# Optimization experiments

Measured on AMD Instinct MI355X. Metric: run time of the kernel, lower is better.

The kernel has to match this reference:

```python
import jax, jax.numpy as jnp
import numpy as np

N_NODES = 100000
N_EDGES = 1600000
D_IN = 128
D_HID = 128
D_OUT = 128


def setup_inputs() -> dict:
    key = jax.random.key(0)
    ks = jax.random.split(key, 6)
    node_features = jax.random.normal(ks[0], (N_NODES, D_IN), dtype=jnp.float32)
    edge_index = jax.random.randint(ks[1], (2, N_EDGES), 0, N_NODES, dtype=jnp.int32)
    s1 = 1.0 / np.sqrt(D_IN)
    s2 = 1.0 / np.sqrt(D_HID)
    W1 = jax.random.normal(ks[2], (D_IN, D_HID), dtype=jnp.float32) * s1
    W2 = jax.random.normal(ks[3], (D_HID, D_HID), dtype=jnp.float32) * s2
    W3 = jax.random.normal(ks[4], (D_HID, D_OUT), dtype=jnp.float32) * s2
    b1 = jnp.zeros((D_HID,), dtype=jnp.float32)
    b2 = jnp.zeros((D_HID,), dtype=jnp.float32)
    b3 = jnp.zeros((D_OUT,), dtype=jnp.float32)
    return {"node_features": node_features, "edge_index": edge_index,
            "W1": W1, "b1": b1, "W2": W2, "b2": b2, "W3": W3, "b3": b3}


def _aggregate(x, src, dst, n_nodes):
    # mean over incoming neighbors (by dst), residual add; degree clamped to >=1
    msg = jax.ops.segment_sum(x[src], dst, num_segments=n_nodes)  # [N, D]
    deg = jax.ops.segment_sum(jnp.ones_like(dst, dtype=x.dtype), dst,
                              num_segments=n_nodes)
    deg = jnp.maximum(deg, 1.0)[:, None]
    return x + msg / deg


def reference(node_features, edge_index, W1, b1, W2, b2, W3, b3):
    n_nodes = node_features.shape[0]
    src, dst = edge_index[0], edge_index[1]
    x = _aggregate(node_features, src, dst, n_nodes)
    x = jax.nn.relu(x @ W1 + b1)
    x = _aggregate(x, src, dst, n_nodes)
    x = jax.nn.relu(x @ W2 + b2)
    x = x.mean(axis=0)  # graph readout -> [D_HID]
    return x @ W3 + b3  # [D_OUT]
```

## Files before the change

kernel.cpp:

```cpp
#include <hip/hip_runtime.h>

#define D 128
#define SLOTS 64
#define NB 391
#define NBANK 8
#define SUBCAP 768
#define BINCAP (NBANK * SUBCAP)
#define BATCH 2048
#define EPB 8
#define CNTSTRIDE 16
#define WPITCH 136

typedef __attribute__((ext_vector_type(8))) short short8;
typedef __attribute__((ext_vector_type(4))) float float4v;

__device__ inline unsigned short f2bf(float f) {
    union { float f; unsigned u; } a; a.f = f;
    unsigned u = a.u;
    return (unsigned short)((u + 0x7fffu + ((u >> 16) & 1u)) >> 16);
}
__device__ inline unsigned packbf(float a, float b) {
    return (unsigned)f2bf(a) | ((unsigned)f2bf(b) << 16);
}
__device__ inline unsigned pack4fp8(float a, float b, float c, float d) {
    int t = __builtin_amdgcn_cvt_pk_fp8_f32(a, b, 0, false);
    t = __builtin_amdgcn_cvt_pk_fp8_f32(c, d, t, true);
    return (unsigned)t;
}
__device__ inline unsigned char pack1fp8(float a) {
    int t = __builtin_amdgcn_cvt_pk_fp8_f32(a, 0.f, 0, false);
    return (unsigned char)(t & 0xff);
}
__device__ inline void acc8fp8(float* acc, uint2 w) {
    auto f0 = __builtin_amdgcn_cvt_pk_f32_fp8(w.x, false);
    auto f1 = __builtin_amdgcn_cvt_pk_f32_fp8(w.x, true);
    auto f2 = __builtin_amdgcn_cvt_pk_f32_fp8(w.y, false);
    auto f3 = __builtin_amdgcn_cvt_pk_f32_fp8(w.y, true);
    acc[0] += f0[0]; acc[1] += f0[1]; acc[2] += f1[0]; acc[3] += f1[1];
    acc[4] += f2[0]; acc[5] += f2[1]; acc[6] += f3[0]; acc[7] += f3[1];
}


__global__ __launch_bounds__(256) void k_head(const int* __restrict__ src,
                                              const int* __restrict__ dst, int nE,
                                              int* __restrict__ gcnt, int* __restrict__ bins,
                                              const float* __restrict__ x,
                                              unsigned char* __restrict__ y8,
                                              unsigned char* __restrict__ h8dummy,
                                              float* __restrict__ colsum,
                                              int n16, int nBatches) {
    __shared__ int hist[512];
    __shared__ int excl[512];
    __shared__ int base[NB];
    __shared__ int stage[BATCH];
    __shared__ int gofs[BATCH];
    __shared__ int waveSum[4];
    int tid = threadIdx.x;

    if (blockIdx.x >= nBatches) {
        int cb = blockIdx.x - nBatches;
        if (cb == 0) {
            if (tid < 128) colsum[tid] = 0.f;
            else if (tid < 136)
                reinterpret_cast<uint4*>(y8)[(size_t)n16 + (tid - 128)] = make_uint4(0, 0, 0, 0);
            else if (tid < 144)
                reinterpret_cast<uint4*>(h8dummy)[tid - 136] = make_uint4(0, 0, 0, 0);
        }
        int i = cb * 256 + tid;
        if (i < n16) {
            const float4* xin = reinterpret_cast<const float4*>(x) + (size_t)i * 4;
            float4 v0 = xin[0], v1 = xin[1], v2 = xin[2], v3 = xin[3];
            uint4 o;
            o.x = pack4fp8(v0.x, v0.y, v0.z, v0.w);
            o.y = pack4fp8(v1.x, v1.y, v1.z, v1.w);
            o.z = pack4fp8(v2.x, v2.y, v2.z, v2.w);
            o.w = pack4fp8(v3.x, v3.y, v3.z, v3.w);
            reinterpret_cast<uint4*>(y8)[i] = o;
        }
        return;
    }

    int start = blockIdx.x * BATCH;
    int cntB = nE - start; if (cntB > BATCH) cntB = BATCH;
    if (cntB <= 0) return;
    int bank = blockIdx.x & (NBANK - 1);

    hist[tid] = 0; hist[tid + 256] = 0;
    __syncthreads();

    int b[EPB], r[EPB], v[EPB];
    #pragma unroll
    for (int i = 0; i < EPB; ++i) {
        int e = start + i * 256 + tid;
        if (e < nE) {
            int d = dst[e];
            b[i] = d >> 8;
            v[i] = (src[e] << 8) | (d & 255);
            r[i] = atomicAdd(&hist[b[i]], 1);
        } else b[i] = -1;
    }
    __syncthreads();

    int e0 = tid * 2, e1 = e0 + 1;
    int h0 = hist[e0], h1v = hist[e1];
    int s = h0 + h1v;
    int lane = tid & 63, w = tid >> 6;
    int sum = s;
    #pragma unroll
    for (int off2 = 1; off2 < 64; off2 <<= 1) {
        int tmp = __shfl_up(sum, off2, 64);
        if (lane >= off2) sum += tmp;
    }
    if (lane == 63) waveSum[w] = sum;
    __syncthreads();
    int wbase = 0;
    if (w > 0) wbase += waveSum[0];
    if (w > 1) wbase += waveSum[1];
    if (w > 2) wbase += waveSum[2];
    int exclPair = wbase + sum - s;
    excl[e0] = exclPair;
    excl[e1] = exclPair + h0;
    if (tid < NB)
        base[tid] = atomicAdd(&gcnt[(tid * NBANK + bank) * CNTSTRIDE], hist[tid]);
    if (tid + 256 < NB)
        base[tid + 256] = atomicAdd(&gcnt[((tid + 256) * NBANK + bank) * CNTSTRIDE], hist[tid + 256]);
    __syncthreads();

    #pragma unroll
    for (int i = 0; i < EPB; ++i) {
        if (b[i] >= 0) {
            int p = excl[b[i]] + r[i];
            int o = base[b[i]] + r[i];
            stage[p] = v[i];
            gofs[p] = (o < SUBCAP) ? (b[i] * BINCAP + bank * SUBCAP + o) : -1;
        }
    }
    __syncthreads();

    #pragma unroll
    for (int i = 0; i < EPB; ++i) {
        int p = i * 256 + tid;
        if (p < cntB) {
            int g = gofs[p];
            if (g >= 0) bins[g] = stage[p];
        }
    }
}


__global__ __launch_bounds__(256) void k_scatter2(const int* __restrict__ gcnt,
                                                  const int* __restrict__ bins,
                                                  int* __restrict__ slots,
                                                  int* __restrict__ deg, int n, int nAll) {
    __shared__ int slotsL[128 * SLOTS];
    __shared__ int cntL[128];
    __shared__ int cnt8s[128];
    int tid = threadIdx.x;
    int bin = blockIdx.x >> 1;
    int half = blockIdx.x & 1;
    if (tid < 128) cntL[tid] = 0;
    __syncthreads();

    #pragma unroll
    for (int k = 0; k < NBANK; ++k) {
        int c = gcnt[(bin * NBANK + k) * CNTSTRIDE]; if (c > SUBCAP) c = SUBCAP;
        const int* eb = bins + (size_t)bin * BINCAP + k * SUBCAP;
        for (int i = tid; i < c; i += 256) {
            int vv = eb[i];
            int dl = vv & 255;
            if ((dl >> 7) == half) {
                int p = atomicAdd(&cntL[dl & 127], 1);
                if (p < SLOTS) slotsL[(dl & 127) * SLOTS + p] = vv >> 8;
            }
        }
    }
    __syncthreads();

    int node0 = bin * 256 + half * 128;
    int remNodes = n - node0;
    if (remNodes > 128) remNodes = 128;
    if (remNodes < 0) remNodes = 0;

    if (tid < remNodes) {
        int dg = cntL[tid]; if (dg > SLOTS) dg = SLOTS;
        int dgr = (dg + 7) & ~7;
        for (int p = dg; p < dgr; ++p) slotsL[tid * SLOTS + p] = nAll;
        deg[node0 + tid] = dg;
        cnt8s[tid] = dgr;
    }
    __syncthreads();

    uint4* gout = reinterpret_cast<uint4*>(slots + (size_t)node0 * SLOTS);
    const uint4* lin = reinterpret_cast<const uint4*>(slotsL);
    int nv = remNodes * (SLOTS / 4);
    for (int i = tid; i < nv; i += 256) {
        int nd = i >> 4, vec = i & 15;
        if ((vec << 2) < cnt8s[nd]) gout[i] = lin[i];
    }
}


__global__ void k_agg(const unsigned char* __restrict__ Xin8,
                      unsigned short* __restrict__ Xout,
                      const int* __restrict__ deg, const int* __restrict__ slots, int n) {
    int t = blockIdx.x * 256 + threadIdx.x;
    int node = t >> 4;
    int lane = t & 15;
    if (node >= n) return;
    int dg = deg[node];
    int cnt8 = (dg + 7) & ~7;
    float acc[8] = {0.f, 0.f, 0.f, 0.f, 0.f, 0.f, 0.f, 0.f};
    const int* sl = slots + (size_t)node * SLOTS;
    for (int j = 0; j < cnt8; j += 8) {
        int4 s4a = *reinterpret_cast<const int4*>(sl + j);
        int4 s4b = *reinterpret_cast<const int4*>(sl + j + 4);
        uint2 w0 = *reinterpret_cast<const uint2*>(Xin8 + (size_t)s4a.x * D + lane * 8);
        uint2 w1 = *reinterpret_cast<const uint2*>(Xin8 + (size_t)s4a.y * D + lane * 8);
        uint2 w2 = *reinterpret_cast<const uint2*>(Xin8 + (size_t)s4a.z * D + lane * 8);
        uint2 w3 = *reinterpret_cast<const uint2*>(Xin8 + (size_t)s4a.w * D + lane * 8);
        uint2 w4 = *reinterpret_cast<const uint2*>(Xin8 + (size_t)s4b.x * D + lane * 8);
        uint2 w5 = *reinterpret_cast<const uint2*>(Xin8 + (size_t)s4b.y * D + lane * 8);
        uint2 w6 = *reinterpret_cast<const uint2*>(Xin8 + (size_t)s4b.z * D + lane * 8);
        uint2 w7 = *reinterpret_cast<const uint2*>(Xin8 + (size_t)s4b.w * D + lane * 8);
        acc8fp8(acc, w0); acc8fp8(acc, w1); acc8fp8(acc, w2); acc8fp8(acc, w3);
        acc8fp8(acc, w4); acc8fp8(acc, w5); acc8fp8(acc, w6); acc8fp8(acc, w7);
    }
    float inv = 1.0f / (float)(dg > 0 ? dg : 1);
    uint2 s8 = *reinterpret_cast<const uint2*>(Xin8 + (size_t)node * D + lane * 8);
    float self[8] = {0.f, 0.f, 0.f, 0.f, 0.f, 0.f, 0.f, 0.f};
    acc8fp8(self, s8);
    float o[8];
    #pragma unroll
    for (int k = 0; k < 8; ++k) o[k] = self[k] + acc[k] * inv;
    uint4 ov;
    ov.x = packbf(o[0], o[1]); ov.y = packbf(o[2], o[3]);
    ov.z = packbf(o[4], o[5]); ov.w = packbf(o[6], o[7]);
    reinterpret_cast<uint4*>(Xout + (size_t)node * D)[lane] = ov;
}


__global__ __launch_bounds__(256) void k_gemm(const unsigned short* __restrict__ X,
                                              const float* __restrict__ W,
                                              const float* __restrict__ bias,
                                              unsigned char* __restrict__ Y8,
                                              float* __restrict__ colsum,
                                              int n, int mode) {
    __shared__ unsigned short Wt[128 * WPITCH];
    __shared__ float cs[128];
    int tid = threadIdx.x;
    int wave = tid >> 6, L = tid & 63;
    int m16 = L & 15, g = L >> 4;

    #pragma unroll
    for (int i = 0; i < 8; ++i) {
        int p = i * 256 + tid;
        int col = p & 127, kg = p >> 7;
        unsigned pk[4];
        #pragma unroll
        for (int h = 0; h < 4; ++h) {
            float w0 = W[(kg * 8 + 2 * h + 0) * 128 + col];
            float w1 = W[(kg * 8 + 2 * h + 1) * 128 + col];
            pk[h] = packbf(w0, w1);
        }
        *reinterpret_cast<uint4*>(&Wt[col * WPITCH + kg * 8]) =
            make_uint4(pk[0], pk[1], pk[2], pk[3]);
    }
    if (mode && tid < 128) cs[tid] = 0.f;
    __syncthreads();

    int row0 = blockIdx.x * 128 + wave * 32;
    float4v zero4 = {0.f, 0.f, 0.f, 0.f};
    float4v acc[2][8];
    #pragma unroll
    for (int rt = 0; rt < 2; ++rt)
        #pragma unroll
        for (int ct = 0; ct < 8; ++ct) acc[rt][ct] = zero4;

    #pragma unroll
    for (int q = 0; q < 4; ++q) {
        int k0 = q * 32;
        short8 a[2];
        #pragma unroll
        for (int rt = 0; rt < 2; ++rt) {
            int row = row0 + rt * 16 + m16;
            short8 af = {0, 0, 0, 0, 0, 0, 0, 0};
            if (row < n)
                af = *reinterpret_cast<const short8*>(X + (size_t)row * D + k0 + g * 8);
            a[rt] = af;
        }
        #pragma unroll
        for (int ct = 0; ct < 8; ++ct) {
            short8 b = *reinterpret_cast<const short8*>(&Wt[(ct * 16 + m16) * WPITCH + k0 + g * 8]);
            acc[0][ct] = __builtin_amdgcn_mfma_f32_16x16x32_bf16(a[0], b, acc[0][ct], 0, 0, 0);
            acc[1][ct] = __builtin_amdgcn_mfma_f32_16x16x32_bf16(a[1], b, acc[1][ct], 0, 0, 0);
        }
    }

    float bj[8];
    #pragma unroll
    for (int ct = 0; ct < 8; ++ct) bj[ct] = bias[ct * 16 + m16];

    if (mode == 0) {
        #pragma unroll
        for (int rt = 0; rt < 2; ++rt)
            #pragma unroll
            for (int i = 0; i < 4; ++i) {
                int row = row0 + rt * 16 + g * 4 + i;
                if (row < n) {
                    #pragma unroll
                    for (int ct = 0; ct < 8; ++ct) {
                        float v = fmaxf(acc[rt][ct][i] + bj[ct], 0.f);
                        Y8[(size_t)row * D + ct * 16 + m16] = pack1fp8(v);
                    }
                }
            }
    } else {
        float csv[8] = {0.f, 0.f, 0.f, 0.f, 0.f, 0.f, 0.f, 0.f};
        #pragma unroll
        for (int rt = 0; rt < 2; ++rt)
            #pragma unroll
            for (int i = 0; i < 4; ++i) {
                int row = row0 + rt * 16 + g * 4 + i;
                if (row < n) {
                    #pragma unroll
                    for (int ct = 0; ct < 8; ++ct)
                        csv[ct] += fmaxf(acc[rt][ct][i] + bj[ct], 0.f);
                }
            }
        #pragma unroll
        for (int ct = 0; ct < 8; ++ct) atomicAdd(&cs[ct * 16 + m16], csv[ct]);
        __syncthreads();
        if (tid < 128) atomicAdd(&colsum[tid], cs[tid]);
    }
}


__global__ void k_final(const float* __restrict__ colsum, const float* __restrict__ W3,
                        const float* __restrict__ b3, float* __restrict__ out, float invN) {
    int j = threadIdx.x;
    float acc = b3[j];
    #pragma unroll 8
    for (int k = 0; k < D; ++k)
        acc += colsum[k] * invN * W3[k * D + j];
    out[j] = acc;
}


extern "C" void kernel_launch(void* const* d_in, const int* in_sizes, int n_in,
                              void* d_out, int out_size, void* d_ws, size_t ws_size,
                              hipStream_t stream) {
    const float* nf = (const float*)d_in[0];
    const int*   ei = (const int*)d_in[1];
    const float* W1 = (const float*)d_in[2];
    const float* b1 = (const float*)d_in[3];
    const float* W2 = (const float*)d_in[4];
    const float* b2 = (const float*)d_in[5];
    const float* W3 = (const float*)d_in[6];
    const float* b3 = (const float*)d_in[7];
    float* out = (float*)d_out;

    int n  = in_sizes[0] / D;
    int nE = in_sizes[1] / 2;
    const int* src = ei;
    const int* dst = ei + nE;

    int nBins = (n + 255) / 256;
    int nBatches = (nE + BATCH - 1) / BATCH;
    int n16 = n * (D / 16);

    char* ws = (char*)d_ws;
    size_t off = 0;
    auto alloc = [&](size_t bytes) -> void* {
        off = (off + 255) & ~(size_t)255;
        void* p = ws + off;
        off += bytes;
        return p;
    };
    int* gcnt  = (int*)alloc((size_t)nBins * NBANK * CNTSTRIDE * 4);
    int* bins  = (int*)alloc((size_t)nBins * BINCAP * 4);
    int* slots = (int*)alloc((size_t)nBins * 256 * SLOTS * 4);
    int* deg   = (int*)alloc((size_t)n * 4);
    unsigned char*  x8  = (unsigned char*) alloc((size_t)(n + 1) * D);
    unsigned short* t16 = (unsigned short*)alloc((size_t)n * D * 2);
    unsigned char*  h8  = (unsigned char*) alloc((size_t)(n + 1) * D);
    float* colsum = (float*)alloc(128 * 4);

    hipMemsetAsync(gcnt, 0, (size_t)nBins * NBANK * CNTSTRIDE * 4, stream);

    int gC = (n16 + 255) / 256;
    int gA = (n * 16 + 255) / 256;
    int gG = (n + 127) / 128;

    k_head<<<nBatches + gC, 256, 0, stream>>>(src, dst, nE, gcnt, bins,
                                              nf, x8, h8 + (size_t)n * D,
                                              colsum, n16, nBatches);
    k_scatter2<<<nBins * 2, 256, 0, stream>>>(gcnt, bins, slots, deg, n, n);

    k_agg<<<gA, 256, 0, stream>>>(x8, t16, deg, slots, n);
    k_gemm<<<gG, 256, 0, stream>>>(t16, W1, b1, h8, (float*)nullptr, n, 0);
    k_agg<<<gA, 256, 0, stream>>>(h8, t16, deg, slots, n);
    k_gemm<<<gG, 256, 0, stream>>>(t16, W2, b2, (unsigned char*)nullptr, colsum, n, 1);
    k_final<<<1, 128, 0, stream>>>(colsum, W3, b3, out, 1.0f / (float)n);
}
```

Before: 250.1 us.

## Halve bucket width to 128 nodes and unroll aggregation gather to 16 neighbors

Edges are now binned into 128-node buckets instead of 256-node buckets, so each scatter block reads only its own bin rather than two blocks each filtering half of a shared bin. That removes the redundant edge reads in the scatter pass. The aggregation kernel now pads neighbor lists to multiples of 16 and issues 16 gathers per iteration for more memory-level parallelism, at the cost of extra padded loads for low-degree nodes. Per-bank capacity shrinks to 448, which raises the risk of dropping edges if a bank overflows.

```diff
diff --git a/kernel.cpp b/kernel.cpp
--- a/kernel.cpp
+++ b/kernel.cpp
@@ -2,9 +2,9 @@
 
 #define D 128
 #define SLOTS 64
-#define NB 391
+#define NB 782
 #define NBANK 8
-#define SUBCAP 768
+#define SUBCAP 448
 #define BINCAP (NBANK * SUBCAP)
 #define BATCH 2048
 #define EPB 8
@@ -49,8 +49,8 @@
                                               unsigned char* __restrict__ h8dummy,
                                               float* __restrict__ colsum,
                                               int n16, int nBatches) {
-    __shared__ int hist[512];
-    __shared__ int excl[512];
+    __shared__ int hist[1024];
+    __shared__ int excl[1024];
     __shared__ int base[NB];
     __shared__ int stage[BATCH];
     __shared__ int gofs[BATCH];
@@ -85,7 +85,7 @@
     if (cntB <= 0) return;
     int bank = blockIdx.x & (NBANK - 1);
 
-    hist[tid] = 0; hist[tid + 256] = 0;
+    hist[tid] = 0; hist[tid + 256] = 0; hist[tid + 512] = 0; hist[tid + 768] = 0;
     __syncthreads();
 
     int b[EPB], r[EPB], v[EPB];
@@ -94,16 +94,16 @@
         int e = start + i * 256 + tid;
         if (e < nE) {
             int d = dst[e];
-            b[i] = d >> 8;
-            v[i] = (src[e] << 8) | (d & 255);
+            b[i] = d >> 7;
+            v[i] = (src[e] << 7) | (d & 127);
             r[i] = atomicAdd(&hist[b[i]], 1);
         } else b[i] = -1;
     }
     __syncthreads();
 
-    int e0 = tid * 2, e1 = e0 + 1;
-    int h0 = hist[e0], h1v = hist[e1];
-    int s = h0 + h1v;
+    int e0 = tid * 4;
+    int h0 = hist[e0], h1v = hist[e0 + 1], h2v = hist[e0 + 2], h3v = hist[e0 + 3];
+    int s = h0 + h1v + h2v + h3v;
     int lane = tid & 63, w = tid >> 6;
     int sum = s;
     #pragma unroll
@@ -117,13 +117,13 @@
     if (w > 0) wbase += waveSum[0];
     if (w > 1) wbase += waveSum[1];
     if (w > 2) wbase += waveSum[2];
-    int exclPair = wbase + sum - s;
-    excl[e0] = exclPair;
-    excl[e1] = exclPair + h0;
-    if (tid < NB)
-        base[tid] = atomicAdd(&gcnt[(tid * NBANK + bank) * CNTSTRIDE], hist[tid]);
-    if (tid + 256 < NB)
-        base[tid + 256] = atomicAdd(&gcnt[((tid + 256) * NBANK + bank) * CNTSTRIDE], hist[tid + 256]);
+    int exclBase = wbase + sum - s;
+    excl[e0] = exclBase;
+    excl[e0 + 1] = exclBase + h0;
+    excl[e0 + 2] = exclBase + h0 + h1v;
+    excl[e0 + 3] = exclBase + h0 + h1v + h2v;
+    for (int bb = tid; bb < NB; bb += 256)
+        base[bb] = atomicAdd(&gcnt[(bb * NBANK + bank) * CNTSTRIDE], hist[bb]);
     __syncthreads();
 
     #pragma unroll
@@ -154,10 +154,9 @@
                                                   int* __restrict__ deg, int n, int nAll) {
     __shared__ int slotsL[128 * SLOTS];
     __shared__ int cntL[128];
-    __shared__ int cnt8s[128];
+    __shared__ int cnt16s[128];
     int tid = threadIdx.x;
-    int bin = blockIdx.x >> 1;
-    int half = blockIdx.x & 1;
+    int bin = blockIdx.x;
     if (tid < 128) cntL[tid] = 0;
     __syncthreads();
 
@@ -167,26 +166,24 @@
         const int* eb = bins + (size_t)bin * BINCAP + k * SUBCAP;
         for (int i = tid; i < c; i += 256) {
             int vv = eb[i];
-            int dl = vv & 255;
-            if ((dl >> 7) == half) {
-                int p = atomicAdd(&cntL[dl & 127], 1);
-                if (p < SLOTS) slotsL[(dl & 127) * SLOTS + p] = vv >> 8;
-            }
-        }
-    }
-    __syncthreads();
-
-    int node0 = bin * 256 + half * 128;
+            int dl = vv & 127;
+            int p = atomicAdd(&cntL[dl], 1);
+            if (p < SLOTS) slotsL[dl * SLOTS + p] = vv >> 7;
+        }
+    }
+    __syncthreads();
+
+    int node0 = bin * 128;
     int remNodes = n - node0;
     if (remNodes > 128) remNodes = 128;
     if (remNodes < 0) remNodes = 0;
 
     if (tid < remNodes) {
         int dg = cntL[tid]; if (dg > SLOTS) dg = SLOTS;
-        int dgr = (dg + 7) & ~7;
+        int dgr = (dg + 15) & ~15;
         for (int p = dg; p < dgr; ++p) slotsL[tid * SLOTS + p] = nAll;
         deg[node0 + tid] = dg;
-        cnt8s[tid] = dgr;
+        cnt16s[tid] = dgr;
     }
     __syncthreads();
 
@@ -195,7 +192,7 @@
     int nv = remNodes * (SLOTS / 4);
     for (int i = tid; i < nv; i += 256) {
         int nd = i >> 4, vec = i & 15;
-        if ((vec << 2) < cnt8s[nd]) gout[i] = lin[i];
+        if ((vec << 2) < cnt16s[nd]) gout[i] = lin[i];
     }
 }
 
@@ -208,25 +205,38 @@
     int lane = t & 15;
     if (node >= n) return;
     int dg = deg[node];
-    int cnt8 = (dg + 7) & ~7;
+    int cnt16 = (dg + 15) & ~15;
     float acc[8] = {0.f, 0.f, 0.f, 0.f, 0.f, 0.f, 0.f, 0.f};
     const int* sl = slots + (size_t)node * SLOTS;
-    for (int j = 0; j < cnt8; j += 8) {
+    const unsigned char* xb = Xin8 + lane * 8;
+    for (int j = 0; j < cnt16; j += 16) {
         int4 s4a = *reinterpret_cast<const int4*>(sl + j);
         int4 s4b = *reinterpret_cast<const int4*>(sl + j + 4);
-        uint2 w0 = *reinterpret_cast<const uint2*>(Xin8 + (size_t)s4a.x * D + lane * 8);
-        uint2 w1 = *reinterpret_cast<const uint2*>(Xin8 + (size_t)s4a.y * D + lane * 8);
-        uint2 w2 = *reinterpret_cast<const uint2*>(Xin8 + (size_t)s4a.z * D + lane * 8);
-        uint2 w3 = *reinterpret_cast<const uint2*>(Xin8 + (size_t)s4a.w * D + lane * 8);
-        uint2 w4 = *reinterpret_cast<const uint2*>(Xin8 + (size_t)s4b.x * D + lane * 8);
-        uint2 w5 = *reinterpret_cast<const uint2*>(Xin8 + (size_t)s4b.y * D + lane * 8);
-        uint2 w6 = *reinterpret_cast<const uint2*>(Xin8 + (size_t)s4b.z * D + lane * 8);
-        uint2 w7 = *reinterpret_cast<const uint2*>(Xin8 + (size_t)s4b.w * D + lane * 8);
+        int4 s4c = *reinterpret_cast<const int4*>(sl + j + 8);
+        int4 s4d = *reinterpret_cast<const int4*>(sl + j + 12);
+        uint2 w0 = *reinterpret_cast<const uint2*>(xb + (size_t)s4a.x * D);
+        uint2 w1 = *reinterpret_cast<const uint2*>(xb + (size_t)s4a.y * D);
+        uint2 w2 = *reinterpret_cast<const uint2*>(xb + (size_t)s4a.z * D);
+        uint2 w3 = *reinterpret_cast<const uint2*>(xb + (size_t)s4a.w * D);
+        uint2 w4 = *reinterpret_cast<const uint2*>(xb + (size_t)s4b.x * D);
+        uint2 w5 = *reinterpret_cast<const uint2*>(xb + (size_t)s4b.y * D);
+        uint2 w6 = *reinterpret_cast<const uint2*>(xb + (size_t)s4b.z * D);
+        uint2 w7 = *reinterpret_cast<const uint2*>(xb + (size_t)s4b.w * D);
+        uint2 w8 = *reinterpret_cast<const uint2*>(xb + (size_t)s4c.x * D);
+        uint2 w9 = *reinterpret_cast<const uint2*>(xb + (size_t)s4c.y * D);
+        uint2 wa = *reinterpret_cast<const uint2*>(xb + (size_t)s4c.z * D);
+        uint2 wb = *reinterpret_cast<const uint2*>(xb + (size_t)s4c.w * D);
+        uint2 wc = *reinterpret_cast<const uint2*>(xb + (size_t)s4d.x * D);
+        uint2 wd = *reinterpret_cast<const uint2*>(xb + (size_t)s4d.y * D);
+        uint2 we = *reinterpret_cast<const uint2*>(xb + (size_t)s4d.z * D);
+        uint2 wf = *reinterpret_cast<const uint2*>(xb + (size_t)s4d.w * D);
         acc8fp8(acc, w0); acc8fp8(acc, w1); acc8fp8(acc, w2); acc8fp8(acc, w3);
         acc8fp8(acc, w4); acc8fp8(acc, w5); acc8fp8(acc, w6); acc8fp8(acc, w7);
+        acc8fp8(acc, w8); acc8fp8(acc, w9); acc8fp8(acc, wa); acc8fp8(acc, wb);
+        acc8fp8(acc, wc); acc8fp8(acc, wd); acc8fp8(acc, we); acc8fp8(acc, wf);
     }
     float inv = 1.0f / (float)(dg > 0 ? dg : 1);
-    uint2 s8 = *reinterpret_cast<const uint2*>(Xin8 + (size_t)node * D + lane * 8);
+    uint2 s8 = *reinterpret_cast<const uint2*>(xb + (size_t)node * D);
     float self[8] = {0.f, 0.f, 0.f, 0.f, 0.f, 0.f, 0.f, 0.f};
     acc8fp8(self, s8);
     float o[8];
@@ -364,7 +374,7 @@
     const int* src = ei;
     const int* dst = ei + nE;
 
-    int nBins = (n + 255) / 256;
+    int nBins = (n + 127) / 128;
     int nBatches = (nE + BATCH - 1) / BATCH;
     int n16 = n * (D / 16);
 
@@ -378,7 +388,7 @@
     };
     int* gcnt  = (int*)alloc((size_t)nBins * NBANK * CNTSTRIDE * 4);
     int* bins  = (int*)alloc((size_t)nBins * BINCAP * 4);
-    int* slots = (int*)alloc((size_t)nBins * 256 * SLOTS * 4);
+    int* slots = (int*)alloc((size_t)nBins * 128 * SLOTS * 4);
     int* deg   = (int*)alloc((size_t)n * 4);
     unsigned char*  x8  = (unsigned char*) alloc((size_t)(n + 1) * D);
     unsigned short* t16 = (unsigned short*)alloc((size_t)n * D * 2);
@@ -394,7 +404,7 @@
     k_head<<<nBatches + gC, 256, 0, stream>>>(src, dst, nE, gcnt, bins,
                                               nf, x8, h8 + (size_t)n * D,
                                               colsum, n16, nBatches);
-    k_scatter2<<<nBins * 2, 256, 0, stream>>>(gcnt, bins, slots, deg, n, n);
+    k_scatter2<<<nBins, 256, 0, stream>>>(gcnt, bins, slots, deg, n, n);
 
     k_agg<<<gA, 256, 0, stream>>>(x8, t16, deg, slots, n);
     k_gemm<<<gG, 256, 0, stream>>>(t16, W1, b1, h8, (float*)nullptr, n, 0);
```

After: 264.4 us. 1.06x slower.
